# Kernel optimization log

Hardware: AMD Instinct MI355X
Metric: run time of the kernel (lower is better)

## Reference

```python
import jax, jax.numpy as jnp
import numpy as np

D_MODEL = 1024
NHEAD = 16
D_K = D_MODEL // NHEAD
SPARSITY = 0.9
DROP_P = 0.1


def setup_inputs() -> dict:
    key = jax.random.key(0)
    ks = jax.random.split(key, 11)
    B, S = 4, 2048
    s = 1.0 / np.sqrt(D_MODEL)
    return {
        "query": jax.random.normal(ks[0], (B, S, D_MODEL), jnp.float32),
        "key": jax.random.normal(ks[1], (B, S, D_MODEL), jnp.float32),
        "value": jax.random.normal(ks[2], (B, S, D_MODEL), jnp.float32),
        "Wq": jax.random.normal(ks[3], (D_MODEL, D_MODEL), jnp.float32) * s,
        "bq": jnp.zeros((D_MODEL,), jnp.float32),
        "Wk": jax.random.normal(ks[4], (D_MODEL, D_MODEL), jnp.float32) * s,
        "bk": jnp.zeros((D_MODEL,), jnp.float32),
        "Wv": jax.random.normal(ks[5], (D_MODEL, D_MODEL), jnp.float32) * s,
        "bv": jnp.zeros((D_MODEL,), jnp.float32),
        "Wo": jax.random.normal(ks[6], (D_MODEL, D_MODEL), jnp.float32) * s,
        "bo": jnp.zeros((D_MODEL,), jnp.float32),
    }


def reference(query, key, value, Wq, bq, Wk, bk, Wv, bv, Wo, bo):
    B, S, _ = query.shape
    # torch Linear: x @ W.T + b
    def proj(x, W, b):
        return (x @ W.T + b).reshape(B, S, NHEAD, D_K).transpose(0, 2, 1, 3)

    Q = proj(query, Wq, bq)   # [B,H,S,d_k]
    K = proj(key, Wk, bk)
    V = proj(value, Wv, bv)

    scores = jnp.einsum("bhqd,bhkd->bhqk", Q, K) / jnp.sqrt(jnp.float32(D_K))
    # random sparsity mask: keep where rand > sparsity (fixed RNG key)
    mkey = jax.random.key(42)
    keep = jax.random.uniform(mkey, scores.shape, jnp.float32) > SPARSITY
    scores = jnp.where(keep, scores, -jnp.inf)
    probs = jax.nn.softmax(scores, axis=-1)
    # dropout on attention probs (train mode, inverted dropout)
    dkey = jax.random.key(7)
    dmask = jax.random.bernoulli(dkey, 1.0 - DROP_P, probs.shape)
    probs = probs * dmask / (1.0 - DROP_P)

    out = jnp.einsum("bhqk,bhkd->bhqd", probs, V)  # [B,H,S,d_k]
    out = out.transpose(0, 2, 1, 3).reshape(B, S, D_MODEL)
    return out @ Wo.T + bo
```

## Files before the change

kernel.cpp:

```cpp
#include <hip/hip_runtime.h>
#include <stdint.h>

typedef unsigned short u16;
typedef unsigned int u32;
typedef __attribute__((ext_vector_type(8))) short short8;
typedef __attribute__((ext_vector_type(4))) float f32x4;

#define DEVI static __device__ __forceinline__

#define S_LEN 2048
#define DMODEL 1024
#define NHEAD 16
#define DK 64
#define NEG_INF (-__builtin_inff())
#define KEEPC 3865470976u
#define DROPC 3865470464u

DEVI u16 f2bf(float f) {
  u32 u = __builtin_bit_cast(u32, f);
  u32 r = u + 0x7fffu + ((u >> 16) & 1u);
  return (u16)(r >> 16);
}

DEVI short8 cvt8(float4 a, float4 b) {
  short8 r;
  r[0] = (short)f2bf(a.x); r[1] = (short)f2bf(a.y);
  r[2] = (short)f2bf(a.z); r[3] = (short)f2bf(a.w);
  r[4] = (short)f2bf(b.x); r[5] = (short)f2bf(b.y);
  r[6] = (short)f2bf(b.z); r[7] = (short)f2bf(b.w);
  return r;
}

DEVI u32 tf_bits(u32 key, u32 i) {
  const u32 K2 = key ^ 0x1BD11BDAu;
  u32 x0 = 0u, x1 = i + key;
#define TFR(r) { x0 += x1; x1 = __builtin_rotateleft32(x1, r); x1 ^= x0; }
  TFR(13) TFR(15) TFR(26) TFR(6)  x0 += key; x1 += K2 + 1u;
  TFR(17) TFR(29) TFR(16) TFR(24) x0 += K2;  x1 += 2u;
  TFR(13) TFR(15) TFR(26) TFR(6)    x1 += key + 3u;
  TFR(17) TFR(29) TFR(16) TFR(24) x0 += key; x1 += K2 + 4u;
  TFR(13) TFR(15) TFR(26) TFR(6)  x0 += K2;  x1 += 5u;
#undef TFR
  return x0 ^ x1;
}

__global__ __launch_bounds__(256) void proj_kernel(
    const float* __restrict__ Xq, const float* __restrict__ Xk, const float* __restrict__ Xv,
    const float* __restrict__ Wq, const float* __restrict__ Wk, const float* __restrict__ Wv,
    const float* __restrict__ bq, const float* __restrict__ bk, const float* __restrict__ bv,
    u16* __restrict__ Qo, u16* __restrict__ Ko, u16* __restrict__ Vto)
{
  const int z = blockIdx.z;
  const float* X = (z == 0) ? Xq : (z == 1) ? Xk : Xv;
  const float* W = (z == 0) ? Wq : (z == 1) ? Wk : Wv;
  const float* bias = (z == 0) ? bq : (z == 1) ? bk : bv;
  const int m0 = blockIdx.x * 64, n0 = blockIdx.y * 64;
  const int tid = threadIdx.x, w = tid >> 6, lane = tid & 63, l = lane & 15, quad = lane >> 4;

  __shared__ __align__(16) u16 lsA[2048], lsB[2048];

  const int srow = tid >> 2, skp = tid & 3;
  const int sc = ((srow >> 4) * 64 + skp * 16 + (srow & 15)) * 8;
  const float* gA = X + (u32)(m0 + srow) * DMODEL + skp * 8;
  const float* gB = W + (u32)(n0 + srow) * DMODEL + skp * 8;

  f32x4 acc[2][2] = {};
  const int mh = (w >> 1) * 2, nh = (w & 1) * 2;

  for (int k0 = 0; k0 < DMODEL; k0 += 32) {
    short8 av  = cvt8(*(const float4*)(gA + k0), *(const float4*)(gA + k0 + 4));
    short8 bv8 = cvt8(*(const float4*)(gB + k0), *(const float4*)(gB + k0 + 4));
    __syncthreads();
    *(short8*)(lsA + sc) = av;
    *(short8*)(lsB + sc) = bv8;
    __syncthreads();
    short8 a0 = *(const short8*)(lsA + ((mh + 0) * 64 + lane) * 8);
    short8 a1 = *(const short8*)(lsA + ((mh + 1) * 64 + lane) * 8);
    short8 b0 = *(const short8*)(lsB + ((nh + 0) * 64 + lane) * 8);
    short8 b1 = *(const short8*)(lsB + ((nh + 1) * 64 + lane) * 8);
    acc[0][0] = __builtin_amdgcn_mfma_f32_16x16x32_bf16(a0, b0, acc[0][0], 0, 0, 0);
    acc[0][1] = __builtin_amdgcn_mfma_f32_16x16x32_bf16(a0, b1, acc[0][1], 0, 0, 0);
    acc[1][0] = __builtin_amdgcn_mfma_f32_16x16x32_bf16(a1, b0, acc[1][0], 0, 0, 0);
    acc[1][1] = __builtin_amdgcn_mfma_f32_16x16x32_bf16(a1, b1, acc[1][1], 0, 0, 0);
  }

  #pragma unroll
  for (int ma = 0; ma < 2; ++ma) {
    #pragma unroll
    for (int nb = 0; nb < 2; ++nb) {
      const int n = n0 + (nh + nb) * 16 + l;
      const float bval = bias[n];
      const int h = n >> 6, d = n & 63;
      #pragma unroll
      for (int r = 0; r < 4; ++r) {
        const int m = m0 + (mh + ma) * 16 + quad * 4 + r;
        float val = acc[ma][nb][r] + bval;
        if (z == 0) val *= 0.125f;
        const int b = m >> 11, s = m & 2047;
        if (z == 0)      Qo [((u32)(b * NHEAD + h) * S_LEN + s) * DK + d] = f2bf(val);
        else if (z == 1) Ko [((u32)(b * NHEAD + h) * S_LEN + s) * DK + d] = f2bf(val);
        else             Vto[((u32)(b * NHEAD + h) * DK + d) * S_LEN + s] = f2bf(val);
      }
    }
  }
}

__global__ __launch_bounds__(256) void attn_kernel(
    const u16* __restrict__ Qs, const u16* __restrict__ Ks, const u16* __restrict__ Vts,
    u16* __restrict__ ctx)
{
  const int qb = blockIdx.x, bh = blockIdx.y;
  const int tid = threadIdx.x, w = tid >> 6, lane = tid & 63, l = lane & 15, quad = lane >> 4;

  __shared__ __align__(16) u16 KPf[4096];
  __shared__ __align__(16) u16 Vf[4096];
  __shared__ __align__(16) u16 dbuf[1024];

  const int qrow0 = qb * 64 + w * 16;
  const u32 qbase = (u32)(bh * S_LEN + qrow0 + l) * DK + quad * 8;
  const short8 qa0 = *(const short8*)(Qs + qbase);
  const short8 qa1 = *(const short8*)(Qs + qbase + 32);

  u32 ibase = ((u32)bh * 2048u + (u32)(qrow0 + quad * 4)) * 2048u + (u32)l;
  const u32 wb0 = ((u32)bh * 2048u + (u32)qrow0) * 2048u;
  const int dwb = w * 256;

  f32x4 o[4] = {};
  float mr[4] = {NEG_INF, NEG_INF, NEG_INF, NEG_INF};
  float lr[4] = {0.f, 0.f, 0.f, 0.f};

  const int kA  = ((tid >> 6) & 3) * 16 + (tid & 15);
  const int kdp = (tid >> 4) & 3;
  const u32 gk  = (u32)(bh * S_LEN + kA) * DK + kdp * 8;
  const int vd  = ((tid >> 7) & 1) * 16 + (tid & 15);
  const int vsp = ((tid >> 6) & 1) * 4 + ((tid >> 4) & 3);
  const u32 gvA = (u32)(bh * DK + vd) * S_LEN + vsp * 8;
  const u32 gvB = (u32)(bh * DK + vd + 32) * S_LEN + vsp * 8;

  const int hi = l >> 3, j = l & 7;
  const int pxor = ((quad >> 1) << 3) | (hi << 4);
  const int pb = (hi * 128 + quad * 32 + j) ^ pxor;
  const int prd = (lane * 8) ^ (lane & 24);
  u16* const pw = KPf + w * 1024;

  for (int kt = 0; kt < 32; ++kt) {
    const u32 ko = (u32)kt * 64u;
    short8 k0v = *(const short8*)(Ks + gk + ko * DK);
    short8 k1v = *(const short8*)(Ks + gk + ko * DK + 32);
    short8 v0v = *(const short8*)(Vts + gvA + ko);
    short8 v1v = *(const short8*)(Vts + gvB + ko);

    u32 m16 = 0;
    #pragma unroll
    for (int c = 0; c < 4; ++c) {
      #pragma unroll
      for (int r = 0; r < 4; ++r) {
        m16 |= (u32)(tf_bits(42u, ibase + (u32)(r * 2048 + c * 16)) >= KEEPC) << (c * 4 + r);
      }
    }
    ibase += 64u;

    const int cnt = __popc(m16);
    int pre = cnt;
    #pragma unroll
    for (int dlt = 1; dlt < 64; dlt <<= 1) {
      int t = __shfl_up(pre, dlt);
      if (lane >= dlt) pre += t;
    }
    const int total = __shfl(pre, 63);
    pre -= cnt;
    {
      u32 mm = m16; int jj = pre;
      while (mm) {
        const u32 s = (u32)__builtin_ctz(mm); mm &= mm - 1u;
        dbuf[dwb + jj] = (u16)(((u32)lane << 4) | s);
        ++jj;
      }
    }
    const u32 wb = wb0 + (u32)kt * 64u;
    for (int ws2 = lane; ws2 < total; ws2 += 64) {
      const u32 e = (u32)dbuf[dwb + ws2];
      const u32 oo = e >> 4, ss = e & 15u;
      const u32 ii = wb + ((oo >> 4) * 4u + (ss & 3u)) * 2048u + (oo & 15u) + (ss >> 2) * 16u;
      const u32 bit = (u32)(tf_bits(7u, ii) < DROPC);
      dbuf[dwb + ws2] = (u16)(e | (bit << 15));
    }
    u32 d16 = 0;
    {
      u32 mm = m16; int jj = pre;
      while (mm) {
        const u32 s = (u32)__builtin_ctz(mm); mm &= mm - 1u;
        d16 |= (u32)((dbuf[dwb + jj] >> 15) & 1u) << s;
        ++jj;
      }
    }

    __syncthreads();
    *(short8*)(KPf + tid * 8) = k0v;
    *(short8*)(KPf + 2048 + tid * 8) = k1v;
    *(short8*)(Vf + tid * 8) = v0v;
    *(short8*)(Vf + 2048 + tid * 8) = v1v;
    __syncthreads();

    f32x4 sc4[4];
    #pragma unroll
    for (int nc = 0; nc < 4; ++nc) {
      short8 kb0 = *(const short8*)(KPf + (nc * 64 + lane) * 8);
      short8 kb1 = *(const short8*)(KPf + ((4 + nc) * 64 + lane) * 8);
      f32x4 zz = {0.f, 0.f, 0.f, 0.f};
      zz = __builtin_amdgcn_mfma_f32_16x16x32_bf16(qa0, kb0, zz, 0, 0, 0);
      sc4[nc] = __builtin_amdgcn_mfma_f32_16x16x32_bf16(qa1, kb1, zz, 0, 0, 0);
    }

    __syncthreads();

    #pragma unroll
    for (int r = 0; r < 4; ++r) {
      float v0 = ((m16 >> (r + 0))  & 1u) ? sc4[0][r] : NEG_INF;
      float v1 = ((m16 >> (r + 4))  & 1u) ? sc4[1][r] : NEG_INF;
      float v2 = ((m16 >> (r + 8))  & 1u) ? sc4[2][r] : NEG_INF;
      float v3 = ((m16 >> (r + 12)) & 1u) ? sc4[3][r] : NEG_INF;
      float mx = fmaxf(fmaxf(v0, v1), fmaxf(v2, v3));
      mx = fmaxf(mx, __shfl_xor(mx, 1));
      mx = fmaxf(mx, __shfl_xor(mx, 2));
      mx = fmaxf(mx, __shfl_xor(mx, 4));
      mx = fmaxf(mx, __shfl_xor(mx, 8));
      const float mn = fmaxf(mr[r], mx);
      const float alpha = (mn == NEG_INF) ? 1.f : __expf(mr[r] - mn);
      mr[r] = mn;
      const float p0 = (v0 == NEG_INF) ? 0.f : __expf(v0 - mn);
      const float p1 = (v1 == NEG_INF) ? 0.f : __expf(v1 - mn);
      const float p2 = (v2 == NEG_INF) ? 0.f : __expf(v2 - mn);
      const float p3 = (v3 == NEG_INF) ? 0.f : __expf(v3 - mn);
      float rs = p0 + p1 + p2 + p3;
      rs += __shfl_xor(rs, 1);
      rs += __shfl_xor(rs, 2);
      rs += __shfl_xor(rs, 4);
      rs += __shfl_xor(rs, 8);
      lr[r] = alpha * lr[r] + rs;
      o[0][r] = o[0][r] * alpha; o[1][r] = o[1][r] * alpha;
      o[2][r] = o[2][r] * alpha; o[3][r] = o[3][r] * alpha;
      const float pd0 = ((d16 >> (r + 0))  & 1u) ? p0 * (1.f / 0.9f) : 0.f;
      const float pd1 = ((d16 >> (r + 4))  & 1u) ? p1 * (1.f / 0.9f) : 0.f;
      const float pd2 = ((d16 >> (r + 8))  & 1u) ? p2 * (1.f / 0.9f) : 0.f;
      const float pd3 = ((d16 >> (r + 12)) & 1u) ? p3 * (1.f / 0.9f) : 0.f;
      const int pi = pb ^ (r * 8);
      pw[pi      ] = f2bf(pd0);
      pw[pi + 256] = f2bf(pd1);
      pw[pi + 512] = f2bf(pd2);
      pw[pi + 768] = f2bf(pd3);
    }
    short8 pa0 = *(const short8*)(pw + prd);
    short8 pa1 = *(const short8*)(pw + 512 + prd);
    #pragma unroll
    for (int nd = 0; nd < 4; ++nd) {
      short8 vb0 = *(const short8*)(Vf + ((nd * 2 + 0) * 64 + lane) * 8);
      short8 vb1 = *(const short8*)(Vf + ((nd * 2 + 1) * 64 + lane) * 8);
      o[nd] = __builtin_amdgcn_mfma_f32_16x16x32_bf16(pa0, vb0, o[nd], 0, 0, 0);
      o[nd] = __builtin_amdgcn_mfma_f32_16x16x32_bf16(pa1, vb1, o[nd], 0, 0, 0);
    }
  }

  const int b = bh >> 4, h = bh & 15;
  #pragma unroll
  for (int r = 0; r < 4; ++r) {
    const float inv = 1.f / lr[r];
    const int qrow = qb * 64 + w * 16 + quad * 4 + r;
    const u32 ob = (u32)(b * S_LEN + qrow) * DMODEL + h * DK;
    ctx[ob + 0  + l] = f2bf(o[0][r] * inv);
    ctx[ob + 16 + l] = f2bf(o[1][r] * inv);
    ctx[ob + 32 + l] = f2bf(o[2][r] * inv);
    ctx[ob + 48 + l] = f2bf(o[3][r] * inv);
  }
}

__global__ __launch_bounds__(256) void oproj_kernel(
    const u16* __restrict__ X, const float* __restrict__ W, const float* __restrict__ bias,
    float* __restrict__ out)
{
  const int m0 = blockIdx.x * 64, n0 = blockIdx.y * 64;
  const int tid = threadIdx.x, w = tid >> 6, lane = tid & 63, l = lane & 15, quad = lane >> 4;

  __shared__ __align__(16) u16 lsA[2048], lsB[2048];

  const int srow = tid >> 2, skp = tid & 3;
  const int sc = ((srow >> 4) * 64 + skp * 16 + (srow & 15)) * 8;
  const u16*  gA = X + (u32)(m0 + srow) * DMODEL + skp * 8;
  const float* gB = W + (u32)(n0 + srow) * DMODEL + skp * 8;

  f32x4 acc[2][2] = {};
  const int mh = (w >> 1) * 2, nh = (w & 1) * 2;

  for (int k0 = 0; k0 < DMODEL; k0 += 32) {
    short8 av  = *(const short8*)(gA + k0);
    short8 bv8 = cvt8(*(const float4*)(gB + k0), *(const float4*)(gB + k0 + 4));
    __syncthreads();
    *(short8*)(lsA + sc) = av;
    *(short8*)(lsB + sc) = bv8;
    __syncthreads();
    short8 a0 = *(const short8*)(lsA + ((mh + 0) * 64 + lane) * 8);
    short8 a1 = *(const short8*)(lsA + ((mh + 1) * 64 + lane) * 8);
    short8 b0 = *(const short8*)(lsB + ((nh + 0) * 64 + lane) * 8);
    short8 b1 = *(const short8*)(lsB + ((nh + 1) * 64 + lane) * 8);
    acc[0][0] = __builtin_amdgcn_mfma_f32_16x16x32_bf16(a0, b0, acc[0][0], 0, 0, 0);
    acc[0][1] = __builtin_amdgcn_mfma_f32_16x16x32_bf16(a0, b1, acc[0][1], 0, 0, 0);
    acc[1][0] = __builtin_amdgcn_mfma_f32_16x16x32_bf16(a1, b0, acc[1][0], 0, 0, 0);
    acc[1][1] = __builtin_amdgcn_mfma_f32_16x16x32_bf16(a1, b1, acc[1][1], 0, 0, 0);
  }

  #pragma unroll
  for (int ma = 0; ma < 2; ++ma) {
    #pragma unroll
    for (int nb = 0; nb < 2; ++nb) {
      const int n = n0 + (nh + nb) * 16 + l;
      const float bval = bias[n];
      #pragma unroll
      for (int r = 0; r < 4; ++r) {
        const int m = m0 + (mh + ma) * 16 + quad * 4 + r;
        out[(u32)m * DMODEL + n] = acc[ma][nb][r] + bval;
      }
    }
  }
}

extern "C" void kernel_launch(void* const* d_in, const int* in_sizes, int n_in,
                              void* d_out, int out_size, void* d_ws, size_t ws_size,
                              hipStream_t stream) {
  (void)in_sizes; (void)n_in; (void)out_size; (void)ws_size;
  const float* q  = (const float*)d_in[0];
  const float* k  = (const float*)d_in[1];
  const float* v  = (const float*)d_in[2];
  const float* Wq = (const float*)d_in[3];
  const float* bq = (const float*)d_in[4];
  const float* Wk = (const float*)d_in[5];
  const float* bk = (const float*)d_in[6];
  const float* Wv = (const float*)d_in[7];
  const float* bv = (const float*)d_in[8];
  const float* Wo = (const float*)d_in[9];
  const float* bo = (const float*)d_in[10];

  char* ws = (char*)d_ws;
  u16* Qs   = (u16*)(ws);
  u16* Ks   = (u16*)(ws + 16777216);
  u16* Vts  = (u16*)(ws + 33554432);
  u16* ctx  = (u16*)(ws + 50331648);

  proj_kernel<<<dim3(128, 16, 3), 256, 0, stream>>>(q, k, v, Wq, Wk, Wv,
                                                    bq, bk, bv, Qs, Ks, Vts);
  attn_kernel<<<dim3(32, 64), 256, 0, stream>>>(Qs, Ks, Vts, ctx);
  oproj_kernel<<<dim3(128, 16), 256, 0, stream>>>(ctx, Wo, bo, (float*)d_out);
}
```

Before: 1.120 ms.

## Software-pipeline attention loop: prefetch next K/V tile and next RNG masks

Restructures the attention main loop so the next tile's K/V global loads are issued right after the current tile is staged into shared memory. The next tile's Threefry keep and dropout masks are computed between the MFMA phases, so the RNG integer work can overlap with matrix ops and memory latency. It also makes the softmax exponentials branchless by clamping the running max instead of testing for -inf. The cost is extra live registers for the prefetched data and masks, and the final iteration's prefetch reads one tile past the end of each head's K/V rows, which can go beyond the buffer for the last head.

```diff
diff --git a/kernel.cpp b/kernel.cpp
--- a/kernel.cpp
+++ b/kernel.cpp
@@ -42,6 +42,54 @@
   TFR(13) TFR(15) TFR(26) TFR(6)  x0 += K2;  x1 += 5u;
 #undef TFR
   return x0 ^ x1;
+}
+
+DEVI u32 keep16(u32 ib) {
+  u32 m16 = 0;
+  #pragma unroll
+  for (int c = 0; c < 4; ++c) {
+    #pragma unroll
+    for (int r = 0; r < 4; ++r) {
+      m16 |= (u32)(tf_bits(42u, ib + (u32)(r * 2048 + c * 16)) >= KEEPC) << (c * 4 + r);
+    }
+  }
+  return m16;
+}
+
+DEVI u32 drop_balanced(u32 m16, u32 wb, int lane, u16* dwp) {
+  const int cnt = __popc(m16);
+  int pre = cnt;
+  #pragma unroll
+  for (int dlt = 1; dlt < 64; dlt <<= 1) {
+    int t = __shfl_up(pre, dlt);
+    if (lane >= dlt) pre += t;
+  }
+  const int total = __shfl(pre, 63);
+  pre -= cnt;
+  {
+    u32 mm = m16; int jj = pre;
+    while (mm) {
+      const u32 s = (u32)__builtin_ctz(mm); mm &= mm - 1u;
+      dwp[jj] = (u16)(((u32)lane << 4) | s);
+      ++jj;
+    }
+  }
+  for (int ws2 = lane; ws2 < total; ws2 += 64) {
+    const u32 e = (u32)dwp[ws2];
+    const u32 oo = e >> 4, ss = e & 15u;
+    const u32 ii = wb + ((oo >> 4) * 4u + (ss & 3u)) * 2048u + (oo & 15u) + (ss >> 2) * 16u;
+    dwp[ws2] = (u16)(e | ((u32)(tf_bits(7u, ii) < DROPC) << 15));
+  }
+  u32 d16 = 0;
+  {
+    u32 mm = m16; int jj = pre;
+    while (mm) {
+      const u32 s = (u32)__builtin_ctz(mm); mm &= mm - 1u;
+      d16 |= (u32)((dwp[jj] >> 15) & 1u) << s;
+      ++jj;
+    }
+  }
+  return d16;
 }
 
 __global__ __launch_bounds__(256) void proj_kernel(
@@ -123,7 +171,7 @@
 
   u32 ibase = ((u32)bh * 2048u + (u32)(qrow0 + quad * 4)) * 2048u + (u32)l;
   const u32 wb0 = ((u32)bh * 2048u + (u32)qrow0) * 2048u;
-  const int dwb = w * 256;
+  u16* const dwp = dbuf + w * 256;
 
   f32x4 o[4] = {};
   float mr[4] = {NEG_INF, NEG_INF, NEG_INF, NEG_INF};
@@ -143,64 +191,29 @@
   const int prd = (lane * 8) ^ (lane & 24);
   u16* const pw = KPf + w * 1024;
 
+  short8 k0v = *(const short8*)(Ks + gk);
+  short8 k1v = *(const short8*)(Ks + gk + 32);
+  short8 v0v = *(const short8*)(Vts + gvA);
+  short8 v1v = *(const short8*)(Vts + gvB);
+  u32 m16 = keep16(ibase);
+  u32 d16 = drop_balanced(m16, wb0, lane, dwp);
+  ibase += 64u;
+
   for (int kt = 0; kt < 32; ++kt) {
-    const u32 ko = (u32)kt * 64u;
-    short8 k0v = *(const short8*)(Ks + gk + ko * DK);
-    short8 k1v = *(const short8*)(Ks + gk + ko * DK + 32);
-    short8 v0v = *(const short8*)(Vts + gvA + ko);
-    short8 v1v = *(const short8*)(Vts + gvB + ko);
-
-    u32 m16 = 0;
-    #pragma unroll
-    for (int c = 0; c < 4; ++c) {
-      #pragma unroll
-      for (int r = 0; r < 4; ++r) {
-        m16 |= (u32)(tf_bits(42u, ibase + (u32)(r * 2048 + c * 16)) >= KEEPC) << (c * 4 + r);
-      }
-    }
-    ibase += 64u;
-
-    const int cnt = __popc(m16);
-    int pre = cnt;
-    #pragma unroll
-    for (int dlt = 1; dlt < 64; dlt <<= 1) {
-      int t = __shfl_up(pre, dlt);
-      if (lane >= dlt) pre += t;
-    }
-    const int total = __shfl(pre, 63);
-    pre -= cnt;
-    {
-      u32 mm = m16; int jj = pre;
-      while (mm) {
-        const u32 s = (u32)__builtin_ctz(mm); mm &= mm - 1u;
-        dbuf[dwb + jj] = (u16)(((u32)lane << 4) | s);
-        ++jj;
-      }
-    }
-    const u32 wb = wb0 + (u32)kt * 64u;
-    for (int ws2 = lane; ws2 < total; ws2 += 64) {
-      const u32 e = (u32)dbuf[dwb + ws2];
-      const u32 oo = e >> 4, ss = e & 15u;
-      const u32 ii = wb + ((oo >> 4) * 4u + (ss & 3u)) * 2048u + (oo & 15u) + (ss >> 2) * 16u;
-      const u32 bit = (u32)(tf_bits(7u, ii) < DROPC);
-      dbuf[dwb + ws2] = (u16)(e | (bit << 15));
-    }
-    u32 d16 = 0;
-    {
-      u32 mm = m16; int jj = pre;
-      while (mm) {
-        const u32 s = (u32)__builtin_ctz(mm); mm &= mm - 1u;
-        d16 |= (u32)((dbuf[dwb + jj] >> 15) & 1u) << s;
-        ++jj;
-      }
-    }
-
     __syncthreads();
     *(short8*)(KPf + tid * 8) = k0v;
     *(short8*)(KPf + 2048 + tid * 8) = k1v;
     *(short8*)(Vf + tid * 8) = v0v;
     *(short8*)(Vf + 2048 + tid * 8) = v1v;
     __syncthreads();
+
+    {
+      const u32 ko = (u32)(kt + 1) * 64u;
+      k0v = *(const short8*)(Ks + gk + ko * DK);
+      k1v = *(const short8*)(Ks + gk + ko * DK + 32);
+      v0v = *(const short8*)(Vts + gvA + ko);
+      v1v = *(const short8*)(Vts + gvB + ko);
+    }
 
     f32x4 sc4[4];
     #pragma unroll
@@ -211,6 +224,7 @@
       zz = __builtin_amdgcn_mfma_f32_16x16x32_bf16(qa0, kb0, zz, 0, 0, 0);
       sc4[nc] = __builtin_amdgcn_mfma_f32_16x16x32_bf16(qa1, kb1, zz, 0, 0, 0);
     }
+    const u32 m16n = keep16(ibase);
 
     __syncthreads();
 
@@ -226,12 +240,13 @@
       mx = fmaxf(mx, __shfl_xor(mx, 4));
       mx = fmaxf(mx, __shfl_xor(mx, 8));
       const float mn = fmaxf(mr[r], mx);
-      const float alpha = (mn == NEG_INF) ? 1.f : __expf(mr[r] - mn);
+      const float mnc = fmaxf(mn, -1e37f);
+      const float alpha = __expf(mr[r] - mnc);
       mr[r] = mn;
-      const float p0 = (v0 == NEG_INF) ? 0.f : __expf(v0 - mn);
-      const float p1 = (v1 == NEG_INF) ? 0.f : __expf(v1 - mn);
-      const float p2 = (v2 == NEG_INF) ? 0.f : __expf(v2 - mn);
-      const float p3 = (v3 == NEG_INF) ? 0.f : __expf(v3 - mn);
+      const float p0 = __expf(v0 - mnc);
+      const float p1 = __expf(v1 - mnc);
+      const float p2 = __expf(v2 - mnc);
+      const float p3 = __expf(v3 - mnc);
       float rs = p0 + p1 + p2 + p3;
       rs += __shfl_xor(rs, 1);
       rs += __shfl_xor(rs, 2);
@@ -259,6 +274,11 @@
       o[nd] = __builtin_amdgcn_mfma_f32_16x16x32_bf16(pa0, vb0, o[nd], 0, 0, 0);
       o[nd] = __builtin_amdgcn_mfma_f32_16x16x32_bf16(pa1, vb1, o[nd], 0, 0, 0);
     }
+
+    u32 d16n = 0;
+    if (kt < 31) d16n = drop_balanced(m16n, wb0 + (u32)(kt + 1) * 64u, lane, dwp);
+    m16 = m16n; d16 = d16n;
+    ibase += 64u;
   }
 
   const int b = bh >> 4, h = bh & 15;
```

New measurement: 1.109 ms, median of 2. Within noise of the previous version (-1.0%).
